# Kernel optimization log

Hardware: AMD Instinct MI355X
Metric: run time of the kernel (lower is better)

## Reference

```python
import jax, jax.numpy as jnp
import numpy as np

B, T, D, H = 4, 2048, 1024, 16
HD = D // H  # 64
FF = 4 * D


def layernorm(x, g, b, eps=1e-5):
    mu = jnp.mean(x, axis=-1, keepdims=True)
    var = jnp.mean(jnp.square(x - mu), axis=-1, keepdims=True)
    return (x - mu) * jax.lax.rsqrt(var + eps) * g + b


def setup_inputs() -> dict:
    key = jax.random.key(0)
    ks = jax.random.split(key, 12)
    s_in = 1.0 / np.sqrt(D)
    s_ff = 1.0 / np.sqrt(FF)
    return {
        "x": jax.random.normal(ks[0], (B, T, D), dtype=jnp.float32),
        "mask": jnp.tril(jnp.ones((T, T), dtype=jnp.int32)),  # causal
        "ln1_g": jnp.ones((D,), jnp.float32),
        "ln1_b": jnp.zeros((D,), jnp.float32),
        "Wq": jax.random.uniform(ks[1], (H, D, HD), jnp.float32, -s_in, s_in),
        "bq": jnp.zeros((H, HD), jnp.float32),
        "Wk": jax.random.uniform(ks[2], (H, D, HD), jnp.float32, -s_in, s_in),
        "bk": jnp.zeros((H, HD), jnp.float32),
        "Wv": jax.random.uniform(ks[3], (H, D, HD), jnp.float32, -s_in, s_in),
        "bv": jnp.zeros((H, HD), jnp.float32),
        "Wo": jax.random.uniform(ks[4], (D, D), jnp.float32, -s_in, s_in),
        "bo": jnp.zeros((D,), jnp.float32),
        "ln2_g": jnp.ones((D,), jnp.float32),
        "ln2_b": jnp.zeros((D,), jnp.float32),
        "W1": jax.random.uniform(ks[5], (D, FF), jnp.float32, -s_in, s_in),
        "b1": jnp.zeros((FF,), jnp.float32),
        "W2": jax.random.uniform(ks[6], (FF, D), jnp.float32, -s_ff, s_ff),
        "b2": jnp.zeros((D,), jnp.float32),
    }


def reference(x, mask, ln1_g, ln1_b, Wq, bq, Wk, bk, Wv, bv, Wo, bo,
              ln2_g, ln2_b, W1, b1, W2, b2):
    # --- attention branch (dropout p=0, eval mode) ---
    h = layernorm(x, ln1_g, ln1_b)                      # [B,T,D]
    q = jnp.einsum('btd,hdk->bhtk', h, Wq) + bq[:, None, :]
    k = jnp.einsum('btd,hdk->bhtk', h, Wk) + bk[:, None, :]
    v = jnp.einsum('btd,hdk->bhtk', h, Wv) + bv[:, None, :]
    scores = jnp.einsum('bhqk,bhsk->bhqs', q, k) / jnp.sqrt(jnp.float32(HD))
    scores = jnp.where(mask == 0, -jnp.inf, scores)     # [B,H,T,T]
    attn = jax.nn.softmax(scores, axis=-1)
    ctx = jnp.einsum('bhqs,bhsk->bhqk', attn, v)        # [B,H,T,HD]
    # concat heads along feature dim (head order preserved)
    ctx = jnp.transpose(ctx, (0, 2, 1, 3)).reshape(x.shape[0], x.shape[1], D)
    attn_out = ctx @ Wo + bo
    x = x + attn_out
    # --- GELU FFN branch (torch nn.GELU default = exact erf) ---
    h2 = layernorm(x, ln2_g, ln2_b)
    ff = jax.nn.gelu(h2 @ W1 + b1, approximate=False) @ W2 + b2
    return x + ff
```

## Files before the change

kernel.cpp:

```cpp
#include <hip/hip_runtime.h>
#include <cstdint>
#include <cstddef>

typedef __bf16 bf16x8 __attribute__((ext_vector_type(8)));
typedef float  floatx4 __attribute__((ext_vector_type(4)));

__device__ __forceinline__ uint16_t f2b(float f) {
    uint32_t u = __builtin_bit_cast(uint32_t, f);
    return (uint16_t)((u + 0x7fffu + ((u >> 16) & 1)) >> 16);
}

__device__ __forceinline__ uint16_t bf16bits(float f) {
    __bf16 h = (__bf16)f;
    return __builtin_bit_cast(uint16_t, h);
}

__device__ __forceinline__ void gload_lds16(const void* g, void* l) {
    __builtin_amdgcn_global_load_lds(
        (__attribute__((address_space(1))) void*)(void*)g,
        (__attribute__((address_space(3))) void*)l, 16, 0, 0);
}

template<int CTRL>
__device__ __forceinline__ float dpp_rot(float v) {
    return __builtin_bit_cast(float,
        __builtin_amdgcn_update_dpp(0, __builtin_bit_cast(int, v),
                                    CTRL, 0xf, 0xf, true));
}
__device__ __forceinline__ float rowmax16(float v) {
    v = fmaxf(v, dpp_rot<0x128>(v));
    v = fmaxf(v, dpp_rot<0x124>(v));
    v = fmaxf(v, dpp_rot<0x122>(v));
    v = fmaxf(v, dpp_rot<0x121>(v));
    return v;
}
__device__ __forceinline__ float rowsum16(float v) {
    v += dpp_rot<0x128>(v);
    v += dpp_rot<0x124>(v);
    v += dpp_rot<0x122>(v);
    v += dpp_rot<0x121>(v);
    return v;
}

#define QSCALE 0.18033688011112042f

__global__ __launch_bounds__(256) void repack_qkv(
    const float* __restrict__ Wq, const float* __restrict__ Wk,
    const float* __restrict__ Wv, uint16_t* __restrict__ out)
{
    __shared__ uint16_t tile[32][33];
    const int m = blockIdx.z >> 4, h = blockIdx.z & 15;
    const float* W = (m == 0) ? Wq : (m == 1) ? Wk : Wv;
    const float scl = (m == 0) ? QSCALE : 1.0f;
    const float* src = W + (size_t)h * 1024 * 64;
    const int d0 = blockIdx.x * 32, hd0 = blockIdx.y * 32;
    const int tx = threadIdx.x & 31, ty = threadIdx.x >> 5;
#pragma unroll
    for (int i = 0; i < 4; ++i)
        tile[ty + i * 8][tx] = f2b(src[(size_t)(d0 + ty + i * 8) * 64 + hd0 + tx] * scl);
    __syncthreads();
    uint16_t* dst = out + (size_t)(m * 1024 + h * 64) * 1024;
#pragma unroll
    for (int i = 0; i < 4; ++i)
        dst[(size_t)(hd0 + ty + i * 8) * 1024 + d0 + tx] = tile[tx][ty + i * 8];
}

__global__ __launch_bounds__(256) void transpose_f2b(
    const float* __restrict__ in, uint16_t* __restrict__ out, int R, int C)
{
    __shared__ uint16_t tile[32][33];
    const int c0 = blockIdx.x * 32, r0 = blockIdx.y * 32;
    const int tx = threadIdx.x & 31, ty = threadIdx.x >> 5;
#pragma unroll
    for (int i = 0; i < 4; ++i)
        tile[ty + i * 8][tx] = f2b(in[(size_t)(r0 + ty + i * 8) * C + c0 + tx]);
    __syncthreads();
#pragma unroll
    for (int i = 0; i < 4; ++i)
        out[(size_t)(c0 + ty + i * 8) * R + r0 + tx] = tile[tx][ty + i * 8];
}

__global__ void concat_bias(const float* __restrict__ bq, const float* __restrict__ bk,
                            const float* __restrict__ bv, float* __restrict__ out)
{
    int i = blockIdx.x * 256 + threadIdx.x;
    out[i] = (i < 1024) ? bq[i] * QSCALE : (i < 2048) ? bk[i - 1024] : bv[i - 2048];
}

__global__ __launch_bounds__(256) void transpose_v(
    const uint16_t* __restrict__ qkv, uint16_t* __restrict__ Vt)
{
    __shared__ uint16_t tile[32][33];
    const int bh = blockIdx.z;
    const int b = bh >> 4, h = bh & 15;
    const int t0 = blockIdx.x * 32, hd0 = blockIdx.y * 32;
    const int tx = threadIdx.x & 31, ty = threadIdx.x >> 5;
    const uint16_t* src = qkv + (size_t)b * 2048 * 3072 + 2048 + h * 64;
#pragma unroll
    for (int i = 0; i < 4; ++i)
        tile[ty + i * 8][tx] = src[(size_t)(t0 + ty + i * 8) * 3072 + hd0 + tx];
    __syncthreads();
    uint16_t* dst = Vt + (size_t)bh * 64 * 2048;
#pragma unroll
    for (int i = 0; i < 4; ++i)
        dst[(size_t)(hd0 + ty + i * 8) * 2048 + t0 + tx] = tile[tx][ty + i * 8];
}

__global__ __launch_bounds__(256) void ln_bf16(
    const float* __restrict__ x, const float* __restrict__ g,
    const float* __restrict__ b, uint16_t* __restrict__ out)
{
    const int row = blockIdx.x;
    const int t = threadIdx.x;
    const float4 v = ((const float4*)(x + (size_t)row * 1024))[t];
    float s  = v.x + v.y + v.z + v.w;
    float s2 = v.x * v.x + v.y * v.y + v.z * v.z + v.w * v.w;
#pragma unroll
    for (int o = 32; o > 0; o >>= 1) { s += __shfl_down(s, o); s2 += __shfl_down(s2, o); }
    __shared__ float red[8];
    const int wave = t >> 6, lane = t & 63;
    if (lane == 0) { red[wave] = s; red[4 + wave] = s2; }
    __syncthreads();
    if (t == 0) {
        float a  = red[0] + red[1] + red[2] + red[3];
        float a2 = red[4] + red[5] + red[6] + red[7];
        float mu = a * (1.0f / 1024.0f);
        red[0] = mu;
        red[4] = rsqrtf(a2 * (1.0f / 1024.0f) - mu * mu + 1e-5f);
    }
    __syncthreads();
    const float mu = red[0], rs = red[4];
    const float4 gv = ((const float4*)g)[t];
    const float4 bv = ((const float4*)b)[t];
    ushort4 ov;
    ov.x = f2b((v.x - mu) * rs * gv.x + bv.x);
    ov.y = f2b((v.y - mu) * rs * gv.y + bv.y);
    ov.z = f2b((v.z - mu) * rs * gv.z + bv.z);
    ov.w = f2b((v.w - mu) * rs * gv.w + bv.w);
    ((ushort4*)(out + (size_t)row * 1024))[t] = ov;
}

__global__ __launch_bounds__(256, 2) void gemm_bf16(
    const uint16_t* __restrict__ A, const uint16_t* __restrict__ Bt,
    int M, int N, int K,
    const float* __restrict__ bias, const float* __restrict__ resid,
    float* __restrict__ outF, uint16_t* __restrict__ outB, int mode)
{
    __shared__ __align__(16) uint16_t lds[128 * 128];
    uint16_t* lA = lds;
    uint16_t* lB = lds + 128 * 32;
    const int tid  = threadIdx.x;
    const int wave = tid >> 6, lane = tid & 63;

    const int lid = (int)blockIdx.y * (int)gridDim.x + (int)blockIdx.x;
    const int xcd = lid & 7, t = lid >> 3;
    const int Mb = (M >> 7) >> 3;
    const int perChunk = Mb * 8;
    const int ch = t / perChunk, j = t - ch * perChunk;
    const int m0 = (xcd * Mb + (j & (Mb - 1))) * 128;
    const int n0 = (ch * 8 + (j / Mb)) * 128;

    const int wm = (wave >> 1) * 64, wn = (wave & 1) * 64;
    const int lrow = lane & 15;
    const int wbase = wave * 64;
    const int lkSw = (((lane >> 4) ^ ((lrow >> 1) & 3))) * 8;

    floatx4 acc[4][4] = {};

    const uint16_t* aT = A  + (size_t)m0 * K;
    const uint16_t* bT = Bt + (size_t)n0 * K;

    for (int k0 = 0; k0 < K; k0 += 32) {
        __syncthreads();
#pragma unroll
        for (int i = 0; i < 2; ++i) {
            const int cw = i * 256 + wbase;
            const int q  = cw + lane;
            const int row = q >> 2;
            const int kc = ((q & 3) ^ ((row >> 1) & 3)) * 8;
            gload_lds16(aT + (size_t)row * K + k0 + kc, &lA[cw * 8]);
            gload_lds16(bT + (size_t)row * K + k0 + kc, &lB[cw * 8]);
        }
        __syncthreads();
        bf16x8 af[4], bfr[4];
#pragma unroll
        for (int mi = 0; mi < 4; ++mi)
            af[mi] = *(const bf16x8*)&lA[(wm + mi * 16 + lrow) * 32 + lkSw];
#pragma unroll
        for (int ni = 0; ni < 4; ++ni)
            bfr[ni] = *(const bf16x8*)&lB[(wn + ni * 16 + lrow) * 32 + lkSw];
#pragma unroll
        for (int mi = 0; mi < 4; ++mi)
#pragma unroll
            for (int ni = 0; ni < 4; ++ni)
                acc[mi][ni] = __builtin_amdgcn_mfma_f32_16x16x32_bf16(
                    af[mi], bfr[ni], acc[mi][ni], 0, 0, 0);
    }

    __syncthreads();
    const int r0 = (lane >> 4) * 4;

    if (mode == 1) {
        float* cf = (float*)lds;
#pragma unroll
        for (int p = 0; p < 2; ++p) {
            if ((wave >> 1) == p) {
#pragma unroll
                for (int ni = 0; ni < 4; ++ni) {
                    const int col = wn + ni * 16 + lrow;
                    const float bv = bias[n0 + col];
#pragma unroll
                    for (int mi = 0; mi < 4; ++mi)
#pragma unroll
                        for (int r = 0; r < 4; ++r) {
                            const int row = mi * 16 + r0 + r;
                            const int g = (col >> 2) ^ (((row >> 2) & 1) << 2);
                            cf[row * 128 + g * 4 + (col & 3)] = acc[mi][ni][r] + bv;
                        }
                }
            }
            __syncthreads();
#pragma unroll
            for (int i = 0; i < 8; ++i) {
                const int ci = i * 256 + tid;
                const int row = ci >> 5, cg = ci & 31;
                const int g = cg ^ (((row >> 2) & 1) << 2);
                float4 v = *(const float4*)&cf[row * 128 + g * 4];
                const size_t gidx = (size_t)(m0 + p * 64 + row) * N + n0 + cg * 4;
                const float4 rz = *(const float4*)&resid[gidx];
                v.x += rz.x; v.y += rz.y; v.z += rz.z; v.w += rz.w;
                *(float4*)&outF[gidx] = v;
            }
            __syncthreads();
        }
    } else {
#pragma unroll
        for (int ni = 0; ni < 4; ++ni) {
            const int col = wn + ni * 16 + lrow;
            const float bv = bias[n0 + col];
#pragma unroll
            for (int mi = 0; mi < 4; ++mi)
#pragma unroll
                for (int r = 0; r < 4; ++r) {
                    const int row = wm + mi * 16 + r0 + r;
                    float v = acc[mi][ni][r] + bv;
                    if (mode == 2)
                        v = 0.5f * v * (1.0f + erff(v * 0.70710678118654752f));
                    const int g = (col >> 3) ^ (((row >> 2) & 3) << 1);
                    lds[row * 128 + g * 8 + (col & 7)] = bf16bits(v);
                }
        }
        __syncthreads();
#pragma unroll
        for (int i = 0; i < 8; ++i) {
            const int ci = i * 256 + tid;
            const int row = ci >> 4, cg = ci & 15;
            const int g = cg ^ (((row >> 2) & 3) << 1);
            const bf16x8 v = *(const bf16x8*)&lds[row * 128 + g * 8];
            *(bf16x8*)&outB[(size_t)(m0 + row) * N + n0 + cg * 8] = v;
        }
    }
}

__global__ __launch_bounds__(256, 2) void attn_kernel(
    const uint16_t* __restrict__ qkv, const uint16_t* __restrict__ Vt,
    uint16_t* __restrict__ ctx)
{
    const int h = blockIdx.y, b = blockIdx.z;
    const int tid = threadIdx.x, wave = tid >> 6, lane = tid & 63;
    const int quad = lane >> 4, lcol = lane & 15, lr4 = quad * 4;
    const int sx = lcol & 7;
    const uint16_t* qbase = qkv + (size_t)b * 2048 * 3072;
    const uint16_t* kgb = qbase + 1024 + h * 64;
    const uint16_t* vtb = Vt + (size_t)(b * 16 + h) * 64 * 2048;

    __shared__ __align__(16) uint16_t kbuf[2][64 * 64];
    __shared__ __align__(16) uint16_t vbuf[2][64 * 64];
    __shared__ __align__(16) uint16_t pshm[4][32 * 64];

    const int rr = lane >> 3, sl = lane & 7;
    const int swz = sl ^ rr;

#define STAGE(ktile, bb)                                                        \
    {                                                                           \
        const int _kb = (ktile) * 64;                                           \
        _Pragma("unroll")                                                       \
        for (int i = 0; i < 2; ++i) {                                           \
            const int j = wave * 2 + i;                                         \
            const int r = j * 8 + rr;                                           \
            gload_lds16(kgb + (size_t)(_kb + r) * 3072 + swz * 8,               \
                        &kbuf[bb][j * 512]);                                    \
            gload_lds16(vtb + (size_t)r * 2048 + _kb + swz * 8,                 \
                        &vbuf[bb][j * 512]);                                    \
        }                                                                       \
    }

    for (int pp = 0; pp < 2; ++pp) {
        const int qt = pp ? (int)blockIdx.x : 15 - (int)blockIdx.x;
        const int qr0 = qt * 128 + wave * 32;

        bf16x8 qf[2][2];
#pragma unroll
        for (int mi = 0; mi < 2; ++mi) {
            const uint16_t* qp = qbase + (size_t)(qr0 + mi * 16 + lcol) * 3072 + h * 64;
            qf[mi][0] = *(const bf16x8*)(qp + quad * 8);
            qf[mi][1] = *(const bf16x8*)(qp + 32 + quad * 8);
        }

        floatx4 o[2][4] = {};
        float m_i[2][4], l_i[2][4];
#pragma unroll
        for (int mi = 0; mi < 2; ++mi)
#pragma unroll
            for (int r = 0; r < 4; ++r) { m_i[mi][r] = -1e30f; l_i[mi][r] = 0.f; }

        const int nk = 2 * qt + 2;
        __syncthreads();
        STAGE(0, 0);
        int cur = 0;

        for (int kt = 0; kt < nk; ++kt) {
            const int kb = kt * 64;
            __syncthreads();
            if (kt + 1 < nk) STAGE(kt + 1, cur ^ 1);

            if (kb <= qr0 + 31) {
                bf16x8 kf[4][2];
#pragma unroll
                for (int nt = 0; nt < 4; ++nt) {
                    const int krow = nt * 16 + lcol;
                    kf[nt][0] = *(const bf16x8*)&kbuf[cur][krow * 64 + ((quad ^ sx) * 8)];
                    kf[nt][1] = *(const bf16x8*)&kbuf[cur][krow * 64 + (((quad + 4) ^ sx) * 8)];
                }
#pragma unroll
                for (int mi = 0; mi < 2; ++mi) {
                    floatx4 sv[4];
#pragma unroll
                    for (int nt = 0; nt < 4; ++nt) {
                        floatx4 s = {0.f, 0.f, 0.f, 0.f};
                        s = __builtin_amdgcn_mfma_f32_16x16x32_bf16(qf[mi][0], kf[nt][0], s, 0, 0, 0);
                        s = __builtin_amdgcn_mfma_f32_16x16x32_bf16(qf[mi][1], kf[nt][1], s, 0, 0, 0);
                        sv[nt] = s;
                    }
                    if (kb + 63 > qr0 + mi * 16) {
#pragma unroll
                        for (int nt = 0; nt < 4; ++nt)
#pragma unroll
                            for (int r = 0; r < 4; ++r) {
                                const int row = qr0 + mi * 16 + lr4 + r;
                                const int col = kb + nt * 16 + lcol;
                                if (col > row) sv[nt][r] = -1e30f;
                            }
                    }
#pragma unroll
                    for (int r = 0; r < 4; ++r) {
                        float m = fmaxf(fmaxf(sv[0][r], sv[1][r]),
                                        fmaxf(sv[2][r], sv[3][r]));
                        m = rowmax16(m);
                        const float mn = fmaxf(m_i[mi][r], m);
                        const float alpha = __builtin_amdgcn_exp2f(m_i[mi][r] - mn);
                        m_i[mi][r] = mn;
                        const int row = mi * 16 + lr4 + r;
                        const int rsw = row & 7;
                        float l = 0.f;
#pragma unroll
                        for (int nt = 0; nt < 4; ++nt) {
                            const float p = __builtin_amdgcn_exp2f(sv[nt][r] - mn);
                            l += p;
                            const int col = nt * 16 + lcol;
                            pshm[wave][row * 64 + (((col >> 3) ^ rsw) * 8) + (col & 7)] =
                                bf16bits(p);
                        }
                        l = rowsum16(l);
                        l_i[mi][r] = l_i[mi][r] * alpha + l;
#pragma unroll
                        for (int ht = 0; ht < 4; ++ht) o[mi][ht][r] *= alpha;
                    }
                }
                bf16x8 pf[2][2];
#pragma unroll
                for (int mi = 0; mi < 2; ++mi) {
                    const int prow = mi * 16 + lcol;
                    pf[mi][0] = *(const bf16x8*)&pshm[wave][prow * 64 + ((quad ^ sx) * 8)];
                    pf[mi][1] = *(const bf16x8*)&pshm[wave][prow * 64 + (((quad + 4) ^ sx) * 8)];
                }
#pragma unroll
                for (int ht = 0; ht < 4; ++ht) {
                    const int hd = ht * 16 + lcol;
                    const bf16x8 vf0 = *(const bf16x8*)&vbuf[cur][hd * 64 + ((quad ^ sx) * 8)];
                    const bf16x8 vf1 = *(const bf16x8*)&vbuf[cur][hd * 64 + (((quad + 4) ^ sx) * 8)];
#pragma unroll
                    for (int mi = 0; mi < 2; ++mi) {
                        o[mi][ht] = __builtin_amdgcn_mfma_f32_16x16x32_bf16(pf[mi][0], vf0, o[mi][ht], 0, 0, 0);
                        o[mi][ht] = __builtin_amdgcn_mfma_f32_16x16x32_bf16(pf[mi][1], vf1, o[mi][ht], 0, 0, 0);
                    }
                }
            }
            cur ^= 1;
        }

#pragma unroll
        for (int mi = 0; mi < 2; ++mi)
#pragma unroll
            for (int r = 0; r < 4; ++r) {
                const float inv = 1.0f / l_i[mi][r];
                const int row = qr0 + mi * 16 + lr4 + r;
#pragma unroll
                for (int ht = 0; ht < 4; ++ht)
                    ctx[(size_t)(b * 2048 + row) * 1024 + h * 64 + ht * 16 + lcol] =
                        bf16bits(o[mi][ht][r] * inv);
            }
    }
#undef STAGE
}

extern "C" void kernel_launch(void* const* d_in, const int* in_sizes, int n_in,
                              void* d_out, int out_size, void* d_ws, size_t ws_size,
                              hipStream_t stream)
{
    (void)in_sizes; (void)n_in; (void)out_size; (void)ws_size;
    const float* x     = (const float*)d_in[0];
    const float* ln1_g = (const float*)d_in[2];
    const float* ln1_b = (const float*)d_in[3];
    const float* Wq    = (const float*)d_in[4];
    const float* bq    = (const float*)d_in[5];
    const float* Wk    = (const float*)d_in[6];
    const float* bk    = (const float*)d_in[7];
    const float* Wv    = (const float*)d_in[8];
    const float* bv    = (const float*)d_in[9];
    const float* Wo    = (const float*)d_in[10];
    const float* bo    = (const float*)d_in[11];
    const float* ln2_g = (const float*)d_in[12];
    const float* ln2_b = (const float*)d_in[13];
    const float* W1    = (const float*)d_in[14];
    const float* b1    = (const float*)d_in[15];
    const float* W2    = (const float*)d_in[16];
    const float* b2    = (const float*)d_in[17];
    float* out = (float*)d_out;

    char* w = (char*)d_ws;
    uint16_t* Wqkv_t = (uint16_t*)w;  w += 6291456;
    uint16_t* Wo_t   = (uint16_t*)w;  w += 2097152;
    uint16_t* W1_t   = (uint16_t*)w;  w += 8388608;
    uint16_t* W2_t   = (uint16_t*)w;  w += 8388608;
    float*    bqkv   = (float*)w;     w += 16384;
    float*    x2     = (float*)w;     w += 33554432;
    char* region = w;
    uint16_t* hbuf = (uint16_t*)region;
    uint16_t* qkv  = (uint16_t*)(region + 16777216);
    uint16_t* Vt   = (uint16_t*)(region + 16777216 + 50331648);
    uint16_t* ctx  = hbuf;
    uint16_t* h2   = (uint16_t*)region;
    uint16_t* a1   = (uint16_t*)(region + 16777216);

    repack_qkv<<<dim3(32, 2, 48), 256, 0, stream>>>(Wq, Wk, Wv, Wqkv_t);
    transpose_f2b<<<dim3(32, 32),  256, 0, stream>>>(Wo, Wo_t, 1024, 1024);
    transpose_f2b<<<dim3(128, 32), 256, 0, stream>>>(W1, W1_t, 1024, 4096);
    transpose_f2b<<<dim3(32, 128), 256, 0, stream>>>(W2, W2_t, 4096, 1024);
    concat_bias<<<12, 256, 0, stream>>>(bq, bk, bv, bqkv);
    ln_bf16<<<8192, 256, 0, stream>>>(x, ln1_g, ln1_b, hbuf);
    gemm_bf16<<<dim3(24, 64), 256, 0, stream>>>(hbuf, Wqkv_t, 8192, 3072, 1024,
                                                bqkv, nullptr, nullptr, qkv, 0);
    transpose_v<<<dim3(64, 2, 64), 256, 0, stream>>>(qkv, Vt);
    attn_kernel<<<dim3(8, 16, 4), 256, 0, stream>>>(qkv, Vt, ctx);
    gemm_bf16<<<dim3(8, 64), 256, 0, stream>>>(ctx, Wo_t, 8192, 1024, 1024,
                                               bo, x, x2, nullptr, 1);
    ln_bf16<<<8192, 256, 0, stream>>>(x2, ln2_g, ln2_b, h2);
    gemm_bf16<<<dim3(32, 64), 256, 0, stream>>>(h2, W1_t, 8192, 4096, 1024,
                                                b1, nullptr, nullptr, a1, 2);
    gemm_bf16<<<dim3(8, 64), 256, 0, stream>>>(a1, W2_t, 8192, 1024, 4096,
                                               b2, x2, out, nullptr, 1);
}
```

Baseline: 567.6 us.

## Double GEMM K-tile to 64 with XOR-swizzled LDS layout and raise occupancy hint

The GEMM main loop now stages a K-slice of 64 instead of 32 per iteration, halving the number of barrier pairs and loop overheads per output tile. The LDS layout switches to a 64-element row with an 8-way XOR swizzle to keep fragment reads conflict-free, and each MFMA pair consumes both halves. The launch-bounds occupancy hint is raised from 2 to 3 blocks per CU, which may constrain registers given the doubled fragment arrays. LDS use stays within the existing 32KB buffer.

```diff
diff --git a/kernel.cpp b/kernel.cpp
--- a/kernel.cpp
+++ b/kernel.cpp
@@ -140,7 +140,7 @@
     ((ushort4*)(out + (size_t)row * 1024))[t] = ov;
 }
 
-__global__ __launch_bounds__(256, 2) void gemm_bf16(
+__global__ __launch_bounds__(256, 3) void gemm_bf16(
     const uint16_t* __restrict__ A, const uint16_t* __restrict__ Bt,
     int M, int N, int K,
     const float* __restrict__ bias, const float* __restrict__ resid,
@@ -148,7 +148,7 @@
 {
     __shared__ __align__(16) uint16_t lds[128 * 128];
     uint16_t* lA = lds;
-    uint16_t* lB = lds + 128 * 32;
+    uint16_t* lB = lds + 128 * 64;
     const int tid  = threadIdx.x;
     const int wave = tid >> 6, lane = tid & 63;
 
@@ -161,40 +161,52 @@
     const int n0 = (ch * 8 + (j / Mb)) * 128;
 
     const int wm = (wave >> 1) * 64, wn = (wave & 1) * 64;
-    const int lrow = lane & 15;
+    const int quad = lane >> 4, lrow = lane & 15;
     const int wbase = wave * 64;
-    const int lkSw = (((lane >> 4) ^ ((lrow >> 1) & 3))) * 8;
 
     floatx4 acc[4][4] = {};
 
     const uint16_t* aT = A  + (size_t)m0 * K;
     const uint16_t* bT = Bt + (size_t)n0 * K;
 
-    for (int k0 = 0; k0 < K; k0 += 32) {
+    for (int k0 = 0; k0 < K; k0 += 64) {
         __syncthreads();
 #pragma unroll
-        for (int i = 0; i < 2; ++i) {
+        for (int i = 0; i < 4; ++i) {
             const int cw = i * 256 + wbase;
             const int q  = cw + lane;
-            const int row = q >> 2;
-            const int kc = ((q & 3) ^ ((row >> 1) & 3)) * 8;
-            gload_lds16(aT + (size_t)row * K + k0 + kc, &lA[cw * 8]);
-            gload_lds16(bT + (size_t)row * K + k0 + kc, &lB[cw * 8]);
+            const int row = q >> 3;
+            const int g = ((q & 7) ^ (row & 7)) * 8;
+            gload_lds16(aT + (size_t)row * K + k0 + g, &lA[cw * 8]);
+            gload_lds16(bT + (size_t)row * K + k0 + g, &lB[cw * 8]);
         }
         __syncthreads();
-        bf16x8 af[4], bfr[4];
+        bf16x8 af[4][2], bfr[4][2];
+#pragma unroll
+        for (int mi = 0; mi < 4; ++mi) {
+            const int rr = wm + mi * 16 + lrow;
+#pragma unroll
+            for (int hh = 0; hh < 2; ++hh)
+                af[mi][hh] = *(const bf16x8*)
+                    &lA[rr * 64 + (((hh * 4 + quad) ^ (rr & 7)) * 8)];
+        }
+#pragma unroll
+        for (int ni = 0; ni < 4; ++ni) {
+            const int rr = wn + ni * 16 + lrow;
+#pragma unroll
+            for (int hh = 0; hh < 2; ++hh)
+                bfr[ni][hh] = *(const bf16x8*)
+                    &lB[rr * 64 + (((hh * 4 + quad) ^ (rr & 7)) * 8)];
+        }
 #pragma unroll
         for (int mi = 0; mi < 4; ++mi)
-            af[mi] = *(const bf16x8*)&lA[(wm + mi * 16 + lrow) * 32 + lkSw];
-#pragma unroll
-        for (int ni = 0; ni < 4; ++ni)
-            bfr[ni] = *(const bf16x8*)&lB[(wn + ni * 16 + lrow) * 32 + lkSw];
-#pragma unroll
-        for (int mi = 0; mi < 4; ++mi)
-#pragma unroll
-            for (int ni = 0; ni < 4; ++ni)
+#pragma unroll
+            for (int ni = 0; ni < 4; ++ni) {
                 acc[mi][ni] = __builtin_amdgcn_mfma_f32_16x16x32_bf16(
-                    af[mi], bfr[ni], acc[mi][ni], 0, 0, 0);
+                    af[mi][0], bfr[ni][0], acc[mi][ni], 0, 0, 0);
+                acc[mi][ni] = __builtin_amdgcn_mfma_f32_16x16x32_bf16(
+                    af[mi][1], bfr[ni][1], acc[mi][ni], 0, 0, 0);
+            }
     }
 
     __syncthreads();
```

Result: faster. 501.6 us (-11.6%).
